# Optimization experiments

Hardware: AMD Instinct MI355X
Metric: run time of the kernel (lower is better)

## Reference

```python
import jax, jax.numpy as jnp
import numpy as np

ROI_SIZE = 7
CROP = ROI_SIZE * 2  # tf crop_and_resize target before 2x2 maxpool


def crop_and_resize(img, boxes, size):
    """TF-semantics bilinear crop_and_resize for a single image.
    img: [H, W, C]; boxes: [N, 4] normalized (y1, x1, y2, x2). -> [N, size, size, C]
    """
    H, W, C = img.shape
    y1, x1, y2, x2 = boxes[:, 0], boxes[:, 1], boxes[:, 2], boxes[:, 3]
    i = jnp.arange(size, dtype=boxes.dtype)
    # TF: in_y = y1*(H-1) + i*(y2-y1)*(H-1)/(size-1)
    ys = y1[:, None] * (H - 1) + i[None, :] * ((y2 - y1)[:, None] * (H - 1) / (size - 1))  # [N,S]
    xs = x1[:, None] * (W - 1) + i[None, :] * ((x2 - x1)[:, None] * (W - 1) / (size - 1))  # [N,S]
    y0 = jnp.floor(ys)
    x0 = jnp.floor(xs)
    wy = (ys - y0)[:, :, None, None]  # [N,S,1,1]
    wx = (xs - x0)[:, None, :, None]  # [N,1,S,1]
    y0i = jnp.clip(y0.astype(jnp.int32), 0, H - 1)
    y1i = jnp.clip(y0i + 1, 0, H - 1)
    x0i = jnp.clip(x0.astype(jnp.int32), 0, W - 1)
    x1i = jnp.clip(x0i + 1, 0, W - 1)

    def gather(yi, xi):  # [N,S],[N,S] -> [N,S,S,C]
        return img[yi[:, :, None], xi[:, None, :]]

    top = gather(y0i, x0i) * (1 - wx) + gather(y0i, x1i) * wx
    bot = gather(y1i, x0i) * (1 - wx) + gather(y1i, x1i) * wx
    return top * (1 - wy) + bot * wy


def setup_inputs() -> dict:
    key = jax.random.key(0)
    ks = jax.random.split(key, 10)
    feats = jax.random.uniform(ks[0], (1, 38, 50, 512), dtype=jnp.float32)  # relu-like feature map
    # valid normalized boxes: sort endpoints per axis
    yy = jnp.sort(jax.random.uniform(ks[1], (1000, 2), dtype=jnp.float32), axis=1)
    xx = jnp.sort(jax.random.uniform(ks[2], (1000, 2), dtype=jnp.float32), axis=1)
    proposals = jnp.stack([yy[:, 0], xx[:, 0], yy[:, 1], xx[:, 1]], axis=1)  # [N,4] y1,x1,y2,x2
    d_flat = ROI_SIZE * ROI_SIZE * 512  # 25088
    W1 = jax.random.normal(ks[3], (d_flat, 4096), dtype=jnp.float32) * 0.01
    b1 = jnp.zeros((4096,), jnp.float32)
    W2 = jax.random.normal(ks[4], (4096, 4096), dtype=jnp.float32) * 0.01
    b2 = jnp.zeros((4096,), jnp.float32)
    Wc = jax.random.normal(ks[5], (4096, 21), dtype=jnp.float32) * 0.01  # class head, stddev 0.01
    bc = jnp.zeros((21,), jnp.float32)
    Wr = jax.random.normal(ks[6], (4096, 80), dtype=jnp.float32) * 0.001  # reg head, stddev 0.001
    br = jnp.zeros((80,), jnp.float32)
    return {"feats": feats, "proposals": proposals, "W1": W1, "b1": b1, "W2": W2,
            "b2": b2, "Wc": Wc, "bc": bc, "Wr": Wr, "br": br}


def reference(feats, proposals, W1, b1, W2, b2, Wc, bc, Wr, br):
    # roi_pool: crop_and_resize to 14x14 (batch_idx all 0), then 2x2 maxpool stride 2 -> 7x7
    rois = crop_and_resize(feats[0], proposals, CROP)  # [N,14,14,C]
    N, _, _, C = rois.shape
    pooled = rois.reshape(N, ROI_SIZE, 2, ROI_SIZE, 2, C).max(axis=(2, 4))  # [N,7,7,C]
    x = pooled.reshape(N, -1)  # flatten (row-major, matches keras Flatten on NHWC)
    x = jax.nn.relu(x @ W1 + b1)
    x = jax.nn.relu(x @ W2 + b2)
    cls_out = jax.nn.softmax(x @ Wc + bc, axis=-1)          # [N, num_classes]
    reg_out = (x @ Wr + br).reshape(N, -1, 4)               # [N, num_classes-1, 4]
    return cls_out, reg_out
```

## Files before the change

kernel.cpp:

```cpp
#include <hip/hip_runtime.h>
#include <stdint.h>

typedef __bf16 bf16x8 __attribute__((ext_vector_type(8)));
typedef float f32x4 __attribute__((ext_vector_type(4)));

__device__ __forceinline__ unsigned short f2bf(float f) {
    unsigned int u = __float_as_uint(f);
    unsigned int r = (u + 0x7fffu + ((u >> 16) & 1u)) >> 16;
    return (unsigned short)r;
}
__device__ __forceinline__ float bf2f(unsigned int h) {
    return __uint_as_float(h << 16);
}

__device__ __forceinline__ void gld_lds16(const void* g, void* l) {
    __builtin_amdgcn_global_load_lds((const __attribute__((address_space(1))) void*)g,
                                     (__attribute__((address_space(3))) void*)l, 16, 0, 0);
}

__global__ __launch_bounds__(256) void k_cvt_feats(const float* __restrict__ src,
                                                   unsigned short* __restrict__ dst) {
    int g = blockIdx.x * 256 + threadIdx.x;
    float4 v = ((const float4*)src)[g];
    ushort4 o;
    o.x = f2bf(v.x); o.y = f2bf(v.y); o.z = f2bf(v.z); o.w = f2bf(v.w);
    ((ushort4*)dst)[g] = o;
}

__global__ __launch_bounds__(256) void k_roipool(const unsigned short* __restrict__ feats,
                                                 const float* __restrict__ props,
                                                 unsigned short* __restrict__ pooled) {
    int b = blockIdx.x;
    int r = b / 49;
    int cell = b - r * 49;
    int py = cell / 7, px = cell - py * 7;
    int c = threadIdx.x * 2;
    unsigned int* outp = (unsigned int*)(pooled + (size_t)r * 25088 + cell * 512 + c);
    if (r >= 1000) { *outp = 0u; return; }
    float y1 = props[r * 4 + 0], x1 = props[r * 4 + 1];
    float y2 = props[r * 4 + 2], x2 = props[r * 4 + 3];
    float sy = (y2 - y1) * (37.0f / 13.0f);
    float sx = (x2 - x1) * (49.0f / 13.0f);
    float m0 = -1e30f, m1 = -1e30f;
#pragma unroll
    for (int a = 0; a < 2; ++a) {
        float ys = y1 * 37.0f + (float)(2 * py + a) * sy;
        float y0f = floorf(ys);
        float wy = ys - y0f;
        int y0 = (int)y0f; y0 = min(max(y0, 0), 37);
        int y1i = min(y0 + 1, 37);
#pragma unroll
        for (int bb = 0; bb < 2; ++bb) {
            float xs = x1 * 49.0f + (float)(2 * px + bb) * sx;
            float x0f = floorf(xs);
            float wx = xs - x0f;
            int x0 = (int)x0f; x0 = min(max(x0, 0), 49);
            int x1i = min(x0 + 1, 49);
            unsigned int t00 = *(const unsigned int*)(feats + ((y0 * 50 + x0) * 512 + c));
            unsigned int t01 = *(const unsigned int*)(feats + ((y0 * 50 + x1i) * 512 + c));
            unsigned int t10 = *(const unsigned int*)(feats + ((y1i * 50 + x0) * 512 + c));
            unsigned int t11 = *(const unsigned int*)(feats + ((y1i * 50 + x1i) * 512 + c));
            float w00 = (1.f - wy) * (1.f - wx), w01 = (1.f - wy) * wx;
            float w10 = wy * (1.f - wx), w11 = wy * wx;
            float v0 = bf2f(t00 & 0xffffu) * w00 + bf2f(t01 & 0xffffu) * w01 +
                       bf2f(t10 & 0xffffu) * w10 + bf2f(t11 & 0xffffu) * w11;
            float v1 = bf2f(t00 >> 16) * w00 + bf2f(t01 >> 16) * w01 +
                       bf2f(t10 >> 16) * w10 + bf2f(t11 >> 16) * w11;
            m0 = fmaxf(m0, v0);
            m1 = fmaxf(m1, v1);
        }
    }
    *outp = ((unsigned int)f2bf(m1) << 16) | (unsigned int)f2bf(m0);
}

__global__ __launch_bounds__(256) void k_transpose_cvt(const float* __restrict__ B,
                                                       unsigned short* __restrict__ BT,
                                                       int K, int N) {
    __shared__ unsigned int tile[64][34];
    int k0 = blockIdx.x * 64;
    int n0 = blockIdx.y * 64;
    int t = threadIdx.x;
    int kr = (t >> 4) * 2;
    int c4 = (t & 15) * 4;
#pragma unroll
    for (int ii = 0; ii < 2; ++ii) {
        int k = kr + ii * 32;
        const float* p0 = B + (size_t)(k0 + k) * N + n0 + c4;
        float4 v0 = *(const float4*)p0;
        float4 v1 = *(const float4*)(p0 + N);
        tile[c4 + 0][k >> 1] = (unsigned)f2bf(v0.x) | ((unsigned)f2bf(v1.x) << 16);
        tile[c4 + 1][k >> 1] = (unsigned)f2bf(v0.y) | ((unsigned)f2bf(v1.y) << 16);
        tile[c4 + 2][k >> 1] = (unsigned)f2bf(v0.z) | ((unsigned)f2bf(v1.z) << 16);
        tile[c4 + 3][k >> 1] = (unsigned)f2bf(v0.w) | ((unsigned)f2bf(v1.w) << 16);
    }
    __syncthreads();
    int nl = t >> 2;
    int kb = (t & 3) * 8;
    uint2 r0 = *(const uint2*)&tile[nl][kb + 0];
    uint2 r1 = *(const uint2*)&tile[nl][kb + 2];
    uint2 r2 = *(const uint2*)&tile[nl][kb + 4];
    uint2 r3 = *(const uint2*)&tile[nl][kb + 6];
    unsigned short* dst = BT + (size_t)(n0 + nl) * K + k0 + (t & 3) * 16;
    *(uint2*)(dst + 0) = r0;
    *(uint2*)(dst + 4) = r1;
    *(uint2*)(dst + 8) = r2;
    *(uint2*)(dst + 12) = r3;
}

__global__ __launch_bounds__(256) void k_gemm(const unsigned short* __restrict__ A,
                                              const unsigned short* __restrict__ BT,
                                              float* __restrict__ Cpart,
                                              int N, int K, int kChunk, int MN) {
    __shared__ __align__(16) unsigned short As[128 * 64];
    __shared__ __align__(16) unsigned short Bs[128 * 64];
    const int n0 = blockIdx.x * 128;
    const int m0 = blockIdx.y * 128;
    const int kBeg = blockIdx.z * kChunk;
    const int kEnd = kBeg + kChunk;
    const int t = threadIdx.x;
    const int lane = t & 63;
    const int wave = t >> 6;
    const int wm = (wave & 1) * 64;
    const int wn = (wave >> 1) * 64;
    const int l15 = lane & 15;
    const int g   = lane >> 4;
    const int xorb = l15 & 7;

    const int srow = t >> 3;
    const int sj = (t & 7) ^ (srow & 7);
    const unsigned short* ag = A + (size_t)(m0 + srow) * K + sj * 8;
    const unsigned short* bg = BT + (size_t)(n0 + srow) * K + sj * 8;
    char* alb = (char*)As + (t & ~63) * 16;
    char* blb = (char*)Bs + (t & ~63) * 16;
    const int rq = K * 32;

    f32x4 acc[4][4] = {};
    const unsigned short* aBase = As + (wm + l15) * 64;
    const unsigned short* bBase = Bs + (wn + l15) * 64;

    for (int kt = kBeg; kt < kEnd; kt += 64) {
#pragma unroll
        for (int q = 0; q < 4; ++q) gld_lds16(ag + kt + q * rq, alb + q * 4096);
#pragma unroll
        for (int q = 0; q < 4; ++q) gld_lds16(bg + kt + q * rq, blb + q * 4096);
        __syncthreads();
#pragma unroll
        for (int s = 0; s < 2; ++s) {
            const int off = ((s * 4 + g) ^ xorb) * 8;
            bf16x8 av[4], bv[4];
#pragma unroll
            for (int i = 0; i < 4; ++i) av[i] = *(const bf16x8*)(aBase + i * 1024 + off);
#pragma unroll
            for (int j = 0; j < 4; ++j) bv[j] = *(const bf16x8*)(bBase + j * 1024 + off);
#pragma unroll
            for (int i = 0; i < 4; ++i)
#pragma unroll
                for (int j = 0; j < 4; ++j)
                    acc[i][j] = __builtin_amdgcn_mfma_f32_16x16x32_bf16(av[i], bv[j], acc[i][j], 0, 0, 0);
        }
        __syncthreads();
    }

    float* Cp = Cpart + (size_t)blockIdx.z * MN;
    const int row_b = m0 + wm + (lane >> 4) * 4;
    const int col_b = n0 + wn + l15;
#pragma unroll
    for (int i = 0; i < 4; ++i)
#pragma unroll
        for (int j = 0; j < 4; ++j)
#pragma unroll
            for (int r = 0; r < 4; ++r)
                Cp[(size_t)(row_b + i * 16 + r) * N + (col_b + j * 16)] = acc[i][j][r];
}

__global__ __launch_bounds__(256) void k_bias_relu_cvt(const float* __restrict__ accP,
                                                       const float* __restrict__ bias,
                                                       unsigned short* __restrict__ out) {
    int gI = blockIdx.x * 256 + threadIdx.x;
    const float4* p = (const float4*)accP;
    float4 v0 = p[gI];
    float4 v1 = p[gI + 1048576];
    float4 v2 = p[gI + 2097152];
    float4 v3 = p[gI + 3145728];
    float4 b = ((const float4*)bias)[gI & 1023];
    ushort4 o;
    o.x = f2bf(fmaxf(v0.x + v1.x + v2.x + v3.x + b.x, 0.f));
    o.y = f2bf(fmaxf(v0.y + v1.y + v2.y + v3.y + b.y, 0.f));
    o.z = f2bf(fmaxf(v0.z + v1.z + v2.z + v3.z + b.z, 0.f));
    o.w = f2bf(fmaxf(v0.w + v1.w + v2.w + v3.w + b.w, 0.f));
    ((ushort4*)out)[gI] = o;
}

__global__ __launch_bounds__(256) void k_pack_w3(const float* __restrict__ Wc,
                                                 const float* __restrict__ Wr,
                                                 unsigned short* __restrict__ W3T) {
    int gI = blockIdx.x * 256 + threadIdx.x;
    int n = gI >> 12, k = gI & 4095;
    float v = 0.f;
    if (n < 21) v = Wc[k * 21 + n];
    else if (n < 101) v = Wr[k * 80 + (n - 21)];
    W3T[gI] = f2bf(v);
}

__global__ __launch_bounds__(64) void k_head(const float* __restrict__ acc3,
                                             const float* __restrict__ bc,
                                             const float* __restrict__ br,
                                             float* __restrict__ out) {
    int r = blockIdx.x;
    int lane = threadIdx.x;
    float logit = -1e30f;
    if (lane < 21) {
        logit = bc[lane];
#pragma unroll
        for (int z = 0; z < 16; ++z) logit += acc3[z * 131072 + r * 128 + lane];
    }
    float mx = logit;
#pragma unroll
    for (int m = 32; m >= 1; m >>= 1) mx = fmaxf(mx, __shfl_xor(mx, m, 64));
    float e = (lane < 21) ? expf(logit - mx) : 0.f;
    float s = e;
#pragma unroll
    for (int m = 32; m >= 1; m >>= 1) s += __shfl_xor(s, m, 64);
    if (lane < 21) out[r * 21 + lane] = e / s;
    for (int j = lane; j < 80; j += 64) {
        float v = br[j];
#pragma unroll
        for (int z = 0; z < 16; ++z) v += acc3[z * 131072 + r * 128 + 21 + j];
        out[21000 + r * 80 + j] = v;
    }
}

extern "C" void kernel_launch(void* const* d_in, const int* in_sizes, int n_in,
                              void* d_out, int out_size, void* d_ws, size_t ws_size,
                              hipStream_t stream) {
    (void)in_sizes; (void)n_in; (void)out_size; (void)ws_size;
    const float* feats = (const float*)d_in[0];
    const float* props = (const float*)d_in[1];
    const float* W1    = (const float*)d_in[2];
    const float* b1    = (const float*)d_in[3];
    const float* W2    = (const float*)d_in[4];
    const float* b2    = (const float*)d_in[5];
    const float* Wc    = (const float*)d_in[6];
    const float* bc    = (const float*)d_in[7];
    const float* Wr    = (const float*)d_in[8];
    const float* br    = (const float*)d_in[9];
    float* out = (float*)d_out;

    char* ws = (char*)d_ws;
    unsigned short* W1T    = (unsigned short*)ws; ws += (size_t)4096 * 25088 * 2;
    unsigned short* W2T    = (unsigned short*)ws; ws += (size_t)4096 * 4096 * 2;
    unsigned short* W3T    = (unsigned short*)ws; ws += (size_t)128 * 4096 * 2;
    unsigned short* featsb = (unsigned short*)ws; ws += (size_t)972800 * 2;
    unsigned short* pooled = (unsigned short*)ws; ws += (size_t)1024 * 25088 * 2;
    unsigned short* x1     = (unsigned short*)ws; ws += (size_t)1024 * 4096 * 2;
    unsigned short* x2     = (unsigned short*)ws; ws += (size_t)1024 * 4096 * 2;
    float* accP            = (float*)ws;          ws += (size_t)4 * 1024 * 4096 * 4;
    float* acc3P           = accP;

    k_cvt_feats<<<950, 256, 0, stream>>>(feats, featsb);
    k_roipool<<<1024 * 49, 256, 0, stream>>>(featsb, props, pooled);
    k_transpose_cvt<<<dim3(392, 64), 256, 0, stream>>>(W1, W1T, 25088, 4096);
    k_gemm<<<dim3(32, 8, 4), 256, 0, stream>>>(pooled, W1T, accP, 4096, 25088, 6272, 1024 * 4096);
    k_bias_relu_cvt<<<4096, 256, 0, stream>>>(accP, b1, x1);
    k_transpose_cvt<<<dim3(64, 64), 256, 0, stream>>>(W2, W2T, 4096, 4096);
    k_gemm<<<dim3(32, 8, 4), 256, 0, stream>>>(x1, W2T, accP, 4096, 4096, 1024, 1024 * 4096);
    k_bias_relu_cvt<<<4096, 256, 0, stream>>>(accP, b2, x2);
    k_pack_w3<<<2048, 256, 0, stream>>>(Wc, Wr, W3T);
    k_gemm<<<dim3(1, 8, 16), 256, 0, stream>>>(x2, W3T, acc3P, 128, 4096, 256, 1024 * 128);
    k_head<<<1000, 64, 0, stream>>>(acc3P, bc, br, out);
}
```

Baseline: 1.076 ms.

## Switch GEMM to 32x32x16 MFMA tiles and swizzle transpose LDS tile

The GEMM inner loop now uses 32x32x16 bf16 MFMA with a 2x2 accumulator grid per wave instead of a 4x4 grid of 16x16x32 MFMAs. Each operand fragment now feeds more math, so LDS reads per FLOP drop, and the epilogue row mapping is rewritten to match the 32x32 output layout. The weight transpose/convert kernel replaces its padded LDS tile with an XOR-swizzled layout and writes 16-byte stores instead of 8-byte ones. The risks are the altered LDS address computation for global_load_lds and a more complex epilogue index pattern.

Result: faster. 997.9 us (-7.3%).

```diff
diff --git a/kernel.cpp b/kernel.cpp
--- a/kernel.cpp
+++ b/kernel.cpp
@@ -2,7 +2,7 @@
 #include <stdint.h>
 
 typedef __bf16 bf16x8 __attribute__((ext_vector_type(8)));
-typedef float f32x4 __attribute__((ext_vector_type(4)));
+typedef float f32x16 __attribute__((ext_vector_type(16)));
 
 __device__ __forceinline__ unsigned short f2bf(float f) {
     unsigned int u = __float_as_uint(f);
@@ -76,7 +76,7 @@
 __global__ __launch_bounds__(256) void k_transpose_cvt(const float* __restrict__ B,
                                                        unsigned short* __restrict__ BT,
                                                        int K, int N) {
-    __shared__ unsigned int tile[64][34];
+    __shared__ unsigned int tile[64][32];
     int k0 = blockIdx.x * 64;
     int n0 = blockIdx.y * 64;
     int t = threadIdx.x;
@@ -85,26 +85,35 @@
 #pragma unroll
     for (int ii = 0; ii < 2; ++ii) {
         int k = kr + ii * 32;
+        int kd = k >> 1;
         const float* p0 = B + (size_t)(k0 + k) * N + n0 + c4;
         float4 v0 = *(const float4*)p0;
         float4 v1 = *(const float4*)(p0 + N);
-        tile[c4 + 0][k >> 1] = (unsigned)f2bf(v0.x) | ((unsigned)f2bf(v1.x) << 16);
-        tile[c4 + 1][k >> 1] = (unsigned)f2bf(v0.y) | ((unsigned)f2bf(v1.y) << 16);
-        tile[c4 + 2][k >> 1] = (unsigned)f2bf(v0.z) | ((unsigned)f2bf(v1.z) << 16);
-        tile[c4 + 3][k >> 1] = (unsigned)f2bf(v0.w) | ((unsigned)f2bf(v1.w) << 16);
+        float lo[4] = {v0.x, v0.y, v0.z, v0.w};
+        float hi[4] = {v1.x, v1.y, v1.z, v1.w};
+#pragma unroll
+        for (int c = 0; c < 4; ++c) {
+            int n = c4 + c;
+            int dw = (((kd >> 1) ^ ((n >> 2) & 7)) << 1) | (kd & 1);
+            tile[n][dw] = (unsigned)f2bf(lo[c]) | ((unsigned)f2bf(hi[c]) << 16);
+        }
     }
     __syncthreads();
     int nl = t >> 2;
-    int kb = (t & 3) * 8;
-    uint2 r0 = *(const uint2*)&tile[nl][kb + 0];
-    uint2 r1 = *(const uint2*)&tile[nl][kb + 2];
-    uint2 r2 = *(const uint2*)&tile[nl][kb + 4];
-    uint2 r3 = *(const uint2*)&tile[nl][kb + 6];
+    int x = (nl >> 2) & 7;
+    int pbase = (t & 3) * 4;
+    uint2 r[4];
+#pragma unroll
+    for (int q = 0; q < 4; ++q) {
+        int p = (pbase + q) ^ x;
+        r[q] = *(const uint2*)&tile[nl][p << 1];
+    }
     unsigned short* dst = BT + (size_t)(n0 + nl) * K + k0 + (t & 3) * 16;
-    *(uint2*)(dst + 0) = r0;
-    *(uint2*)(dst + 4) = r1;
-    *(uint2*)(dst + 8) = r2;
-    *(uint2*)(dst + 12) = r3;
+    uint4 o0, o1;
+    o0.x = r[0].x; o0.y = r[0].y; o0.z = r[1].x; o0.w = r[1].y;
+    o1.x = r[2].x; o1.y = r[2].y; o1.z = r[3].x; o1.w = r[3].y;
+    *(uint4*)(dst + 0) = o0;
+    *(uint4*)(dst + 8) = o1;
 }
 
 __global__ __launch_bounds__(256) void k_gemm(const unsigned short* __restrict__ A,
@@ -122,21 +131,21 @@
     const int wave = t >> 6;
     const int wm = (wave & 1) * 64;
     const int wn = (wave >> 1) * 64;
-    const int l15 = lane & 15;
-    const int g   = lane >> 4;
-    const int xorb = l15 & 7;
+    const int l31 = lane & 31;
+    const int half = lane >> 5;
+    const int xorb = l31 & 7;
 
     const int srow = t >> 3;
     const int sj = (t & 7) ^ (srow & 7);
     const unsigned short* ag = A + (size_t)(m0 + srow) * K + sj * 8;
     const unsigned short* bg = BT + (size_t)(n0 + srow) * K + sj * 8;
-    char* alb = (char*)As + (t & ~63) * 16;
-    char* blb = (char*)Bs + (t & ~63) * 16;
+    char* alb = (char*)As + t * 16;
+    char* blb = (char*)Bs + t * 16;
     const int rq = K * 32;
 
-    f32x4 acc[4][4] = {};
-    const unsigned short* aBase = As + (wm + l15) * 64;
-    const unsigned short* bBase = Bs + (wn + l15) * 64;
+    f32x16 acc[2][2] = {};
+    const unsigned short* aBase = As + (wm + l31) * 64;
+    const unsigned short* bBase = Bs + (wn + l31) * 64;
 
     for (int kt = kBeg; kt < kEnd; kt += 64) {
 #pragma unroll
@@ -145,32 +154,32 @@
         for (int q = 0; q < 4; ++q) gld_lds16(bg + kt + q * rq, blb + q * 4096);
         __syncthreads();
 #pragma unroll
-        for (int s = 0; s < 2; ++s) {
-            const int off = ((s * 4 + g) ^ xorb) * 8;
-            bf16x8 av[4], bv[4];
-#pragma unroll
-            for (int i = 0; i < 4; ++i) av[i] = *(const bf16x8*)(aBase + i * 1024 + off);
-#pragma unroll
-            for (int j = 0; j < 4; ++j) bv[j] = *(const bf16x8*)(bBase + j * 1024 + off);
-#pragma unroll
-            for (int i = 0; i < 4; ++i)
-#pragma unroll
-                for (int j = 0; j < 4; ++j)
-                    acc[i][j] = __builtin_amdgcn_mfma_f32_16x16x32_bf16(av[i], bv[j], acc[i][j], 0, 0, 0);
+        for (int s = 0; s < 4; ++s) {
+            const int off = ((s * 2 + half) ^ xorb) * 8;
+            bf16x8 a0 = *(const bf16x8*)(aBase + off);
+            bf16x8 a1 = *(const bf16x8*)(aBase + 2048 + off);
+            bf16x8 b0 = *(const bf16x8*)(bBase + off);
+            bf16x8 b1 = *(const bf16x8*)(bBase + 2048 + off);
+            acc[0][0] = __builtin_amdgcn_mfma_f32_32x32x16_bf16(a0, b0, acc[0][0], 0, 0, 0);
+            acc[0][1] = __builtin_amdgcn_mfma_f32_32x32x16_bf16(a0, b1, acc[0][1], 0, 0, 0);
+            acc[1][0] = __builtin_amdgcn_mfma_f32_32x32x16_bf16(a1, b0, acc[1][0], 0, 0, 0);
+            acc[1][1] = __builtin_amdgcn_mfma_f32_32x32x16_bf16(a1, b1, acc[1][1], 0, 0, 0);
         }
         __syncthreads();
     }
 
     float* Cp = Cpart + (size_t)blockIdx.z * MN;
-    const int row_b = m0 + wm + (lane >> 4) * 4;
-    const int col_b = n0 + wn + l15;
-#pragma unroll
-    for (int i = 0; i < 4; ++i)
-#pragma unroll
-        for (int j = 0; j < 4; ++j)
-#pragma unroll
-            for (int r = 0; r < 4; ++r)
-                Cp[(size_t)(row_b + i * 16 + r) * N + (col_b + j * 16)] = acc[i][j][r];
+    const int colb = n0 + wn + l31;
+    const int rbase = m0 + wm + 4 * half;
+#pragma unroll
+    for (int i = 0; i < 2; ++i)
+#pragma unroll
+        for (int j = 0; j < 2; ++j)
+#pragma unroll
+            for (int reg = 0; reg < 16; ++reg) {
+                int row = rbase + i * 32 + (reg & 3) + 8 * (reg >> 2);
+                Cp[(size_t)row * N + colb + j * 32] = acc[i][j][reg];
+            }
 }
 
 __global__ __launch_bounds__(256) void k_bias_relu_cvt(const float* __restrict__ accP,
```
